# Optimization experiments

Hardware: AMD Instinct MI355X
Metric: run time of the kernel (lower is better)

Reference implementation:

```python
import jax, jax.numpy as jnp
import numpy as np
from jax import lax

S = 48          # fixed crop size (original crops are ragged; fixed here for batching)
EPS = 0.1       # Sinkhorn entropic regularization
ITERS = 50      # Sinkhorn iterations
TINY = 1e-8


def setup_inputs() -> dict:
    key = jax.random.key(0)
    k1, k2, k3 = jax.random.split(key, 3)
    B, C, H, W = 16, 5, 160, 160
    hm_gt = jax.random.uniform(k1, (B, C, H, W), dtype=jnp.float32)
    hm_pred = jax.random.uniform(k2, (B, C, H, W), dtype=jnp.float32)
    tops = jax.random.randint(k3, (B, 8, 2), 0, 112, dtype=jnp.int32)  # (y, x) per rect
    return {"hm_gt": hm_gt, "hm_pred": hm_pred, "tops": tops}


def _geometry_distance(s):
    # pairwise Euclidean distance between pixel centers of an s x s crop -> [s*s, s*s]
    ys, xs = jnp.meshgrid(jnp.arange(s, dtype=jnp.float32),
                          jnp.arange(s, dtype=jnp.float32), indexing="ij")
    pts = jnp.stack([ys.ravel(), xs.ravel()], axis=-1)          # [s*s, 2]
    d2 = jnp.sum((pts[:, None, :] - pts[None, :, :]) ** 2, -1)  # [s*s, s*s]
    return jnp.sqrt(d2)


def _crop_all(hm, tops):
    # hm: [B, C, H, W], tops: [B, R, 2] -> crops [B, R, C, S, S]
    def crop_one(hm_b, top):  # hm_b [C,H,W], top [2]
        return lax.dynamic_slice(hm_b, (0, top[0], top[1]), (hm_b.shape[0], S, S))
    return jax.vmap(lambda hb, tb: jax.vmap(lambda t: crop_one(hb, t))(tb))(hm, tops)


def reference(hm_gt, hm_pred, tops):
    B, C, H, W = hm_gt.shape
    n = S * S
    dist = _geometry_distance(S)            # [n, n]
    K = jnp.exp(-dist / EPS)                # Gibbs kernel
    M = K * dist                            # for the transport cost readout

    a = _crop_all(hm_gt, tops).reshape(-1, n)    # [N, n]
    b = _crop_all(hm_pred, tops).reshape(-1, n)  # [N, n]
    a = a / (jnp.sum(a, -1, keepdims=True) + TINY)   # normalize to marginals
    b = b / (jnp.sum(b, -1, keepdims=True) + TINY)

    N = a.shape[0]
    u0 = jnp.full((N, n), 1.0 / n, dtype=a.dtype)
    v0 = jnp.full((N, n), 1.0 / n, dtype=a.dtype)

    def body(carry, _):
        u, v = carry
        v = b / (u @ K + TINY)      # [N,n] @ [n,n]
        u = a / (v @ K.T + TINY)
        return (u, v), None

    (u, v), _ = lax.scan(body, (u0, v0), None, length=ITERS)
    # loss per crop: sum_ij u_i K_ij dist_ij v_j
    loss = jnp.sum((u @ M) * v)
    return loss
```

## Files before the change

### kernel.cpp

```cpp
#include <hip/hip_runtime.h>

#define TINYF 1e-8f
#define NITER 50

__device__ __forceinline__ float bperm(int addr4, float v) {
    return __int_as_float(__builtin_amdgcn_ds_bpermute(addr4, __float_as_int(v)));
}
__device__ __forceinline__ float dpp_shr1(float v) {
    return __int_as_float(__builtin_amdgcn_update_dpp(0, __float_as_int(v), 0x111, 0xf, 0xf, true));
}
__device__ __forceinline__ float dpp_shl1(float v) {
    return __int_as_float(__builtin_amdgcn_update_dpp(0, __float_as_int(v), 0x101, 0xf, 0xf, true));
}

#define PREPF(C0_, C1_, C2_) \
    L2 = dpp_shr1(C1_); L1 = dpp_shr1(C2_); R1 = dpp_shl1(C0_); R2 = dpp_shl1(C1_); \
    s1a = L1 + C1_; s1b = C0_ + C2_; s1c = C1_ + R1; \
    s2a = L2 + C2_; s2b = L1 + R1; s2c = C0_ + R2;
#define PREPS(C0_, C1_, C2_) \
    L1 = dpp_shr1(C2_); R1 = dpp_shl1(C0_); \
    s1a = L1 + C1_; s1b = C0_ + C2_; s1c = C1_ + R1;
#define AT0(I, C0_, C1_, C2_, KA, KB, KC) \
    acc[I][0] += KA * C0_ + KB * s1a + KC * s2a; \
    acc[I][1] += KA * C1_ + KB * s1b + KC * s2b; \
    acc[I][2] += KA * C2_ + KB * s1c + KC * s2c;
#define AT1(I, C0_, C1_, C2_, KA, KB) \
    acc[I][0] += KA * C0_ + KB * s1a; \
    acc[I][1] += KA * C1_ + KB * s1b; \
    acc[I][2] += KA * C2_ + KB * s1c;
#define AT2(I, C0_, C1_, C2_, KA) \
    acc[I][0] += KA * C0_; \
    acc[I][1] += KA * C1_; \
    acc[I][2] += KA * C2_;

__global__ void __launch_bounds__(128)
__attribute__((amdgpu_waves_per_eu(1, 2)))
sinkhorn_t13r(const float* __restrict__ hm_gt,
              const float* __restrict__ hm_pred,
              const int* __restrict__ tops,
              float* __restrict__ out) {
    __shared__ __align__(16) float EX[2 * 512];
    __shared__ float sred[4];

    const int t = threadIdx.x;
    const int W = t >> 6;
    const int l = t & 63;
    const int b = l >> 4, c = l & 15;
    const bool btop = (b == 0), bbot = (b == 3);
    const bool xchg = (W == 0) ? bbot : btop;
    const int upA = ((l - 16) & 63) << 2;
    const int dnA = ((l + 16) & 63) << 2;

    const int blk = blockIdx.x;
    const int bi = blk / 40, rr = (blk / 5) % 8, cc = blk % 5;
    const int y0 = tops[(bi * 8 + rr) * 2 + 0];
    const int x0 = tops[(bi * 8 + rr) * 2 + 1];
    const float* srcA = hm_gt + (size_t)(bi * 5 + cc) * 25600;
    const float* srcB = hm_pred + (size_t)(bi * 5 + cc) * 25600;

    float* wp = EX + W * 256 + c * 4;
    const float* rp = EX + (1 - W) * 256 + c * 4;

    float va[6][3], vb[6][3];
    float sA = 0.f, sB = 0.f;
    const int rbase = y0 + 24 * W + 6 * b;
#pragma unroll
    for (int i = 0; i < 6; ++i) {
        const int g = (rbase + i) * 160 + x0 + 3 * c;
#pragma unroll
        for (int j = 0; j < 3; ++j) {
            const float A = srcA[g + j];
            const float B = srcB[g + j];
            va[i][j] = A; vb[i][j] = B;
            sA += A; sB += B;
        }
    }
#pragma unroll
    for (int o = 1; o < 64; o <<= 1) {
        sA += __shfl_xor(sA, o, 64);
        sB += __shfl_xor(sB, o, 64);
    }
    if (l == 0) { sred[W] = sA; sred[2 + W] = sB; }
    __syncthreads();
    sA = sred[0] + sred[1];
    sB = sred[2] + sred[3];
    const float nA = 1.0f / (sA + TINYF);
    const float nB = 1.0f / (sB + TINYF);
#pragma unroll
    for (int i = 0; i < 6; ++i)
#pragma unroll
        for (int j = 0; j < 3; ++j) { va[i][j] *= nA; vb[i][j] *= nB; }

    const float e10 = expf(-1.0f / 0.1f);
    const float e2  = expf(-sqrtf(2.0f) / 0.1f);
    const float e20 = expf(-2.0f / 0.1f);

    float xu[6][3], xv[6][3], acc[6][3];
    const float u0 = 1.0f / 2304.0f;
#pragma unroll
    for (int i = 0; i < 6; ++i)
#pragma unroll
        for (int j = 0; j < 3; ++j) xu[i][j] = u0;

    if (xchg) {
        *(float4*)(wp)      = make_float4(u0, u0, u0, 0.f);
        *(float4*)(wp + 64) = make_float4(u0, u0, u0, 0.f);
    }
    __syncthreads();

    auto conv = [&](const float (&x)[6][3], int poffR,
                    float K00, float K01, float K02,
                    float K10, float K11, float K20) {
        float4 q0 = make_float4(0.f, 0.f, 0.f, 0.f), q1 = q0;
        if (xchg) {
            q0 = *(const float4*)(rp + poffR);
            q1 = *(const float4*)(rp + poffR + 64);
        }
        float tA[3], tB[3], tC[3], tD[3];
#pragma unroll
        for (int j = 0; j < 3; ++j) {
            tA[j] = bperm(upA, x[4][j]);
            tB[j] = bperm(upA, x[5][j]);
            tC[j] = bperm(dnA, x[0][j]);
            tD[j] = bperm(dnA, x[1][j]);
        }
#pragma unroll
        for (int i = 0; i < 6; ++i)
#pragma unroll
            for (int j = 0; j < 3; ++j) acc[i][j] = 0.f;

        float L1, L2, R1, R2, s1a, s1b, s1c, s2a, s2b, s2c;
#pragma unroll
        for (int w = 0; w < 6; ++w) {
            PREPF(x[w][0], x[w][1], x[w][2])
            if (w >= 2) { AT2(w - 2, x[w][0], x[w][1], x[w][2], K20) }
            if (w >= 1) { AT1(w - 1, x[w][0], x[w][1], x[w][2], K10, K11) }
            { AT0(w, x[w][0], x[w][1], x[w][2], K00, K01, K02) }
            if (w <= 4) { AT1(w + 1, x[w][0], x[w][1], x[w][2], K10, K11) }
            if (w <= 3) { AT2(w + 2, x[w][0], x[w][1], x[w][2], K20) }
        }
        float hA[3], hB[3], hC[3], hD[3];
        const float qv0[3] = {q0.x, q0.y, q0.z};
        const float qv1[3] = {q1.x, q1.y, q1.z};
#pragma unroll
        for (int j = 0; j < 3; ++j) {
            if (W == 0) {
                hA[j] = btop ? 0.f : tA[j];
                hB[j] = btop ? 0.f : tB[j];
                hC[j] = bbot ? qv0[j] : tC[j];
                hD[j] = bbot ? qv1[j] : tD[j];
            } else {
                hA[j] = btop ? qv0[j] : tA[j];
                hB[j] = btop ? qv1[j] : tB[j];
                hC[j] = bbot ? 0.f : tC[j];
                hD[j] = bbot ? 0.f : tD[j];
            }
        }
        PREPS(hB[0], hB[1], hB[2])
        { AT1(0, hB[0], hB[1], hB[2], K10, K11) }
        { AT2(1, hB[0], hB[1], hB[2], K20) }
        { AT2(0, hA[0], hA[1], hA[2], K20) }
        PREPS(hC[0], hC[1], hC[2])
        { AT2(4, hC[0], hC[1], hC[2], K20) }
        { AT1(5, hC[0], hC[1], hC[2], K10, K11) }
        { AT2(5, hD[0], hD[1], hD[2], K20) }
    };

    auto publish = [&](const float (&y)[6][3], int poffW) {
        if (xchg) {
            const int r0 = (W == 0) ? 4 : 0;
            *(float4*)(wp + poffW)      = make_float4(y[r0][0], y[r0][1], y[r0][2], 0.f);
            *(float4*)(wp + poffW + 64) = make_float4(y[r0+1][0], y[r0+1][1], y[r0+1][2], 0.f);
        }
        __syncthreads();
    };

#pragma unroll 1
    for (int it = 0; it < NITER; ++it) {
        conv(xu, 0, 1.0f, e10, e20, e10, e2, e20);
#pragma unroll
        for (int i = 0; i < 6; ++i)
#pragma unroll
            for (int j = 0; j < 3; ++j)
                xv[i][j] = vb[i][j] * __builtin_amdgcn_rcpf(acc[i][j] + TINYF);
        publish(xv, 512);

        conv(xv, 512, 1.0f, e10, e20, e10, e2, e20);
#pragma unroll
        for (int i = 0; i < 6; ++i)
#pragma unroll
            for (int j = 0; j < 3; ++j)
                xu[i][j] = va[i][j] * __builtin_amdgcn_rcpf(acc[i][j] + TINYF);
        publish(xu, 0);
    }

    const float s2f = sqrtf(2.0f);
    const float m01 = e10, m02 = e20 * 2.0f, m11 = e2 * s2f;
    conv(xu, 0, 0.0f, m01, m02, m01, m11, m02);
    float lsum = 0.f;
#pragma unroll
    for (int i = 0; i < 6; ++i)
#pragma unroll
        for (int j = 0; j < 3; ++j)
            lsum += acc[i][j] * xv[i][j];

#pragma unroll
    for (int o = 1; o < 64; o <<= 1) lsum += __shfl_xor(lsum, o, 64);
    if (l == 0) sred[W] = lsum;
    __syncthreads();
    if (t == 0) atomicAdd(out, sred[0] + sred[1]);
}

extern "C" void kernel_launch(void* const* d_in, const int* in_sizes, int n_in,
                              void* d_out, int out_size, void* d_ws, size_t ws_size,
                              hipStream_t stream) {
    (void)in_sizes; (void)n_in; (void)out_size; (void)d_ws; (void)ws_size;
    const float* hm_gt = (const float*)d_in[0];
    const float* hm_pred = (const float*)d_in[1];
    const int* tops = (const int*)d_in[2];
    float* out = (float*)d_out;

    hipMemsetAsync(out, 0, sizeof(float), stream);
    sinkhorn_t13r<<<dim3(640), dim3(128), 0, stream>>>(hm_gt, hm_pred, tops, out);
}
```

Baseline: 184.8 us.

## Split each crop across four waves with 3-row strips per lane

Each 48x48 crop is now processed by four wavefronts (256 threads) instead of two, so every lane owns a 3x3 patch rather than 6x3. Halo rows are exchanged through shared memory between all adjacent waves, using dummy zeroed slots for the outer boundary so the edge logic has no branches. This halves the per-thread convolution work and register footprint on the serial 50-iteration critical path. In exchange, every lane at a strip edge now does LDS halo writes and reads, and each barrier synchronises four waves instead of two.

```diff
diff --git a/kernel.cpp b/kernel.cpp
--- a/kernel.cpp
+++ b/kernel.cpp
@@ -2,6 +2,7 @@
 
 #define TINYF 1e-8f
 #define NITER 50
+#define EXN 2304
 
 __device__ __forceinline__ float bperm(int addr4, float v) {
     return __int_as_float(__builtin_amdgcn_ds_bpermute(addr4, __float_as_int(v)));
@@ -33,21 +34,21 @@
     acc[I][1] += KA * C1_; \
     acc[I][2] += KA * C2_;
 
-__global__ void __launch_bounds__(128)
+__global__ void __launch_bounds__(256)
 __attribute__((amdgpu_waves_per_eu(1, 2)))
-sinkhorn_t13r(const float* __restrict__ hm_gt,
-              const float* __restrict__ hm_pred,
-              const int* __restrict__ tops,
-              float* __restrict__ out) {
-    __shared__ __align__(16) float EX[2 * 512];
-    __shared__ float sred[4];
+sinkhorn_q4(const float* __restrict__ hm_gt,
+            const float* __restrict__ hm_pred,
+            const int* __restrict__ tops,
+            float* __restrict__ out) {
+    __shared__ __align__(16) float EX[EXN];
+    __shared__ float sred[8];
 
     const int t = threadIdx.x;
-    const int W = t >> 6;
+    const int w = t >> 6;
     const int l = t & 63;
-    const int b = l >> 4, c = l & 15;
-    const bool btop = (b == 0), bbot = (b == 3);
-    const bool xchg = (W == 0) ? bbot : btop;
+    const int lr = l >> 4, c = l & 15;
+    const bool b0 = (lr == 0), b3 = (lr == 3);
+    const bool edge = b0 || b3;
     const int upA = ((l - 16) & 63) << 2;
     const int dnA = ((l + 16) & 63) << 2;
 
@@ -58,14 +59,21 @@
     const float* srcA = hm_gt + (size_t)(bi * 5 + cc) * 25600;
     const float* srcB = hm_pred + (size_t)(bi * 5 + cc) * 25600;
 
-    float* wp = EX + W * 256 + c * 4;
-    const float* rp = EX + (1 - W) * 256 + c * 4;
-
-    float va[6][3], vb[6][3];
+    const int rs = b0 ? ((w - 1) * 2 + 1) : ((w + 1) * 2 + 0);
+    const bool rvalid = (b0 && w > 0) || (b3 && w < 3);
+    const float* rp0 = EX + (rvalid ? rs * 128 + c * 4 : 2048 + c * 4);
+    const float* rp1 = EX + (rvalid ? 1024 + rs * 128 + c * 4 : 2048 + c * 4);
+    const int wslot = w * 2 + (b0 ? 0 : 1);
+    float* wp0 = EX + (edge ? wslot * 128 + c * 4 : 2176 + c * 4);
+    float* wp1 = EX + (edge ? 1024 + wslot * 128 + c * 4 : 2176 + c * 4);
+
+    for (int p = t; p < EXN; p += 256) EX[p] = 0.f;
+
+    float va[3][3], vb[3][3];
     float sA = 0.f, sB = 0.f;
-    const int rbase = y0 + 24 * W + 6 * b;
-#pragma unroll
-    for (int i = 0; i < 6; ++i) {
+    const int rbase = y0 + 12 * w + 3 * lr;
+#pragma unroll
+    for (int i = 0; i < 3; ++i) {
         const int g = (rbase + i) * 160 + x0 + 3 * c;
 #pragma unroll
         for (int j = 0; j < 3; ++j) {
@@ -80,14 +88,14 @@
         sA += __shfl_xor(sA, o, 64);
         sB += __shfl_xor(sB, o, 64);
     }
-    if (l == 0) { sred[W] = sA; sred[2 + W] = sB; }
+    if (l == 0) { sred[w] = sA; sred[4 + w] = sB; }
     __syncthreads();
-    sA = sred[0] + sred[1];
-    sB = sred[2] + sred[3];
+    sA = sred[0] + sred[1] + sred[2] + sred[3];
+    sB = sred[4] + sred[5] + sred[6] + sred[7];
     const float nA = 1.0f / (sA + TINYF);
     const float nB = 1.0f / (sB + TINYF);
 #pragma unroll
-    for (int i = 0; i < 6; ++i)
+    for (int i = 0; i < 3; ++i)
 #pragma unroll
         for (int j = 0; j < 3; ++j) { va[i][j] *= nA; vb[i][j] *= nB; }
 
@@ -95,120 +103,115 @@
     const float e2  = expf(-sqrtf(2.0f) / 0.1f);
     const float e20 = expf(-2.0f / 0.1f);
 
-    float xu[6][3], xv[6][3], acc[6][3];
+    float xu[3][3], xv[3][3], acc[3][3];
     const float u0 = 1.0f / 2304.0f;
 #pragma unroll
-    for (int i = 0; i < 6; ++i)
+    for (int i = 0; i < 3; ++i)
 #pragma unroll
         for (int j = 0; j < 3; ++j) xu[i][j] = u0;
 
-    if (xchg) {
-        *(float4*)(wp)      = make_float4(u0, u0, u0, 0.f);
-        *(float4*)(wp + 64) = make_float4(u0, u0, u0, 0.f);
-    }
+    *(float4*)(wp0)      = make_float4(u0, u0, u0, 0.f);
+    *(float4*)(wp0 + 64) = make_float4(u0, u0, u0, 0.f);
     __syncthreads();
 
-    auto conv = [&](const float (&x)[6][3], int poffR,
+    auto conv = [&](const float (&x)[3][3], const float* rpo,
                     float K00, float K01, float K02,
                     float K10, float K11, float K20) {
-        float4 q0 = make_float4(0.f, 0.f, 0.f, 0.f), q1 = q0;
-        if (xchg) {
-            q0 = *(const float4*)(rp + poffR);
-            q1 = *(const float4*)(rp + poffR + 64);
-        }
+        const float4 q0 = *(const float4*)(rpo);
+        const float4 q1 = *(const float4*)(rpo + 64);
         float tA[3], tB[3], tC[3], tD[3];
 #pragma unroll
         for (int j = 0; j < 3; ++j) {
-            tA[j] = bperm(upA, x[4][j]);
-            tB[j] = bperm(upA, x[5][j]);
+            tA[j] = bperm(upA, x[1][j]);
+            tB[j] = bperm(upA, x[2][j]);
             tC[j] = bperm(dnA, x[0][j]);
             tD[j] = bperm(dnA, x[1][j]);
         }
 #pragma unroll
-        for (int i = 0; i < 6; ++i)
+        for (int i = 0; i < 3; ++i)
 #pragma unroll
             for (int j = 0; j < 3; ++j) acc[i][j] = 0.f;
 
         float L1, L2, R1, R2, s1a, s1b, s1c, s2a, s2b, s2c;
-#pragma unroll
-        for (int w = 0; w < 6; ++w) {
-            PREPF(x[w][0], x[w][1], x[w][2])
-            if (w >= 2) { AT2(w - 2, x[w][0], x[w][1], x[w][2], K20) }
-            if (w >= 1) { AT1(w - 1, x[w][0], x[w][1], x[w][2], K10, K11) }
-            { AT0(w, x[w][0], x[w][1], x[w][2], K00, K01, K02) }
-            if (w <= 4) { AT1(w + 1, x[w][0], x[w][1], x[w][2], K10, K11) }
-            if (w <= 3) { AT2(w + 2, x[w][0], x[w][1], x[w][2], K20) }
-        }
+        PREPF(x[0][0], x[0][1], x[0][2])
+        AT0(0, x[0][0], x[0][1], x[0][2], K00, K01, K02)
+        AT1(1, x[0][0], x[0][1], x[0][2], K10, K11)
+        AT2(2, x[0][0], x[0][1], x[0][2], K20)
+        PREPF(x[1][0], x[1][1], x[1][2])
+        AT1(0, x[1][0], x[1][1], x[1][2], K10, K11)
+        AT0(1, x[1][0], x[1][1], x[1][2], K00, K01, K02)
+        AT1(2, x[1][0], x[1][1], x[1][2], K10, K11)
+        PREPF(x[2][0], x[2][1], x[2][2])
+        AT2(0, x[2][0], x[2][1], x[2][2], K20)
+        AT1(1, x[2][0], x[2][1], x[2][2], K10, K11)
+        AT0(2, x[2][0], x[2][1], x[2][2], K00, K01, K02)
+
         float hA[3], hB[3], hC[3], hD[3];
         const float qv0[3] = {q0.x, q0.y, q0.z};
         const float qv1[3] = {q1.x, q1.y, q1.z};
 #pragma unroll
         for (int j = 0; j < 3; ++j) {
-            if (W == 0) {
-                hA[j] = btop ? 0.f : tA[j];
-                hB[j] = btop ? 0.f : tB[j];
-                hC[j] = bbot ? qv0[j] : tC[j];
-                hD[j] = bbot ? qv1[j] : tD[j];
-            } else {
-                hA[j] = btop ? qv0[j] : tA[j];
-                hB[j] = btop ? qv1[j] : tB[j];
-                hC[j] = bbot ? 0.f : tC[j];
-                hD[j] = bbot ? 0.f : tD[j];
-            }
+            hA[j] = b0 ? qv0[j] : tA[j];
+            hB[j] = b0 ? qv1[j] : tB[j];
+            hC[j] = b3 ? qv0[j] : tC[j];
+            hD[j] = b3 ? qv1[j] : tD[j];
         }
         PREPS(hB[0], hB[1], hB[2])
-        { AT1(0, hB[0], hB[1], hB[2], K10, K11) }
-        { AT2(1, hB[0], hB[1], hB[2], K20) }
-        { AT2(0, hA[0], hA[1], hA[2], K20) }
+        AT1(0, hB[0], hB[1], hB[2], K10, K11)
+        AT2(1, hB[0], hB[1], hB[2], K20)
+        AT2(0, hA[0], hA[1], hA[2], K20)
         PREPS(hC[0], hC[1], hC[2])
-        { AT2(4, hC[0], hC[1], hC[2], K20) }
-        { AT1(5, hC[0], hC[1], hC[2], K10, K11) }
-        { AT2(5, hD[0], hD[1], hD[2], K20) }
+        AT2(1, hC[0], hC[1], hC[2], K20)
+        AT1(2, hC[0], hC[1], hC[2], K10, K11)
+        AT2(2, hD[0], hD[1], hD[2], K20)
     };
 
-    auto publish = [&](const float (&y)[6][3], int poffW) {
-        if (xchg) {
-            const int r0 = (W == 0) ? 4 : 0;
-            *(float4*)(wp + poffW)      = make_float4(y[r0][0], y[r0][1], y[r0][2], 0.f);
-            *(float4*)(wp + poffW + 64) = make_float4(y[r0+1][0], y[r0+1][1], y[r0+1][2], 0.f);
-        }
+    auto publish = [&](const float (&y)[3][3], float* wpo) {
+        const float f0 = b0 ? y[0][0] : y[1][0];
+        const float f1 = b0 ? y[0][1] : y[1][1];
+        const float f2 = b0 ? y[0][2] : y[1][2];
+        const float g0 = b0 ? y[1][0] : y[2][0];
+        const float g1 = b0 ? y[1][1] : y[2][1];
+        const float g2 = b0 ? y[1][2] : y[2][2];
+        *(float4*)(wpo)      = make_float4(f0, f1, f2, 0.f);
+        *(float4*)(wpo + 64) = make_float4(g0, g1, g2, 0.f);
         __syncthreads();
     };
 
 #pragma unroll 1
     for (int it = 0; it < NITER; ++it) {
-        conv(xu, 0, 1.0f, e10, e20, e10, e2, e20);
-#pragma unroll
-        for (int i = 0; i < 6; ++i)
+        conv(xu, rp0, 1.0f, e10, e20, e10, e2, e20);
+#pragma unroll
+        for (int i = 0; i < 3; ++i)
 #pragma unroll
             for (int j = 0; j < 3; ++j)
                 xv[i][j] = vb[i][j] * __builtin_amdgcn_rcpf(acc[i][j] + TINYF);
-        publish(xv, 512);
-
-        conv(xv, 512, 1.0f, e10, e20, e10, e2, e20);
-#pragma unroll
-        for (int i = 0; i < 6; ++i)
+        publish(xv, wp1);
+
+        conv(xv, rp1, 1.0f, e10, e20, e10, e2, e20);
+#pragma unroll
+        for (int i = 0; i < 3; ++i)
 #pragma unroll
             for (int j = 0; j < 3; ++j)
                 xu[i][j] = va[i][j] * __builtin_amdgcn_rcpf(acc[i][j] + TINYF);
-        publish(xu, 0);
+        publish(xu, wp0);
     }
 
     const float s2f = sqrtf(2.0f);
     const float m01 = e10, m02 = e20 * 2.0f, m11 = e2 * s2f;
-    conv(xu, 0, 0.0f, m01, m02, m01, m11, m02);
+    conv(xu, rp0, 0.0f, m01, m02, m01, m11, m02);
     float lsum = 0.f;
 #pragma unroll
-    for (int i = 0; i < 6; ++i)
+    for (int i = 0; i < 3; ++i)
 #pragma unroll
         for (int j = 0; j < 3; ++j)
             lsum += acc[i][j] * xv[i][j];
 
 #pragma unroll
     for (int o = 1; o < 64; o <<= 1) lsum += __shfl_xor(lsum, o, 64);
-    if (l == 0) sred[W] = lsum;
+    if (l == 0) sred[w] = lsum;
     __syncthreads();
-    if (t == 0) atomicAdd(out, sred[0] + sred[1]);
+    if (t == 0) atomicAdd(out, sred[0] + sred[1] + sred[2] + sred[3]);
 }
 
 extern "C" void kernel_launch(void* const* d_in, const int* in_sizes, int n_in,
@@ -221,5 +224,5 @@
     float* out = (float*)d_out;
 
     hipMemsetAsync(out, 0, sizeof(float), stream);
-    sinkhorn_t13r<<<dim3(640), dim3(128), 0, stream>>>(hm_gt, hm_pred, tops, out);
-}
+    sinkhorn_q4<<<dim3(640), dim3(256), 0, stream>>>(hm_gt, hm_pred, tops, out);
+}
```

New measurement: 208.9 us. 1.13x slower.
